# Performance work log

Hardware: AMD Instinct MI355X
Metric: run time of the kernel (lower is better)

## Reference

```python
import jax, jax.numpy as jnp
import numpy as np

EPS = 1e-12  # torch F.normalize default eps


def setup_inputs() -> dict:
    key = jax.random.key(0)
    ks = jax.random.split(key, 4)
    b, c, h, w = 2, 192, 256, 256
    num_heads = 4
    x = jax.random.normal(ks[0], (b, c, h, w), dtype=jnp.float32)
    w_qkv = jax.random.normal(ks[1], (3 * c, c), dtype=jnp.float32) * 0.02
    w_dw = jax.random.normal(ks[2], (3 * c, 1, 3, 3), dtype=jnp.float32) * 0.1
    w_proj = jax.random.normal(ks[3], (c, c), dtype=jnp.float32) * 0.02
    temperature = jnp.ones((num_heads, 1, 1), dtype=jnp.float32)
    return {"x": x, "w_qkv": w_qkv, "w_dw": w_dw, "w_proj": w_proj,
            "temperature": temperature, "num_heads": num_heads}


def reference(x, w_qkv, w_dw, w_proj, temperature, num_heads):
    b, c, h, w = x.shape
    ch = c // num_heads
    # 1x1 conv (pointwise GEMM) then depthwise 3x3 conv
    qkv = jnp.einsum('bchw,oc->bohw', x, w_qkv)
    qkv = jax.lax.conv_general_dilated(
        qkv, w_dw, window_strides=(1, 1), padding='SAME',
        dimension_numbers=('NCHW', 'OIHW', 'NCHW'),
        feature_group_count=3 * c)
    q, k, v = jnp.split(qkv, 3, axis=1)
    # b (head c) h w -> b head (c h) w
    def to_heads(t):
        return t.reshape(b, num_heads, ch * h, w)
    q, k, v = to_heads(q), to_heads(k), to_heads(v)
    # L2-normalize over the (c h) axis
    def l2n(t):
        n = jnp.sqrt(jnp.sum(t * t, axis=-2, keepdims=True))
        return t / jnp.maximum(n, EPS)
    q, k = l2n(q), l2n(k)
    # channel-transposed attention over width: attn is (b, head, w, w)
    attn = jnp.einsum('bhcw,bhcv->bhwv', q, k) * temperature[None]
    attn = jax.nn.softmax(attn, axis=-2)  # softmax over dim=-2 as in source
    out = jnp.einsum('bhcw,bhwv->bhcv', v, attn)
    out = out.reshape(b, c, h, w)
    return jnp.einsum('bchw,oc->bohw', out, w_proj)
```

## Files before the change

kernel.cpp:

```cpp
#include <hip/hip_runtime.h>
#include <math.h>

#define HW 65536

typedef float f32x4 __attribute__((ext_vector_type(4)));
typedef short bf16x8 __attribute__((ext_vector_type(8)));
typedef short bf16x4 __attribute__((ext_vector_type(4)));

static constexpr size_t OFF_A0    = 0;
static constexpr size_t OFF_SP    = 100663296;
static constexpr size_t OFF_QKT   = 150994944;
static constexpr size_t OFF_VPL   = 251658240;
static constexpr size_t OFF_PT    = 301989888;
static constexpr size_t OFF_NORMS = 303038464;
static constexpr size_t OFF_WQ    = 303054848;
static constexpr size_t OFF_WP    = 303276032;

__device__ inline float b2f(unsigned short u) { union { unsigned u; float f; } v; v.u = ((unsigned)u) << 16; return v.f; }
__device__ inline unsigned short f2b(float f) {
    union { float f; unsigned u; } v; v.f = f;
    return (unsigned short)((v.u + 0x7fffu + ((v.u >> 16) & 1u)) >> 16);
}

__global__ __launch_bounds__(256) void conv_w(const float* __restrict__ wq, const float* __restrict__ wp,
                                              unsigned short* __restrict__ wqb, unsigned short* __restrict__ wpb)
{
    int t = blockIdx.x * 256 + threadIdx.x;
    int stride = gridDim.x * 256;
    for (int i = t; i < 576 * 192; i += stride) wqb[i] = f2b(wq[i]);
    for (int i = t; i < 192 * 192; i += stride) wpb[i] = f2b(wp[i]);
}

template <int MODE>
__global__ __launch_bounds__(256) void gemm_pm5(const unsigned short* __restrict__ Aw,
                                                const void* __restrict__ Bsrc,
                                                unsigned short* __restrict__ outb,
                                                float* __restrict__ outf, int Mtiles)
{
    __shared__ unsigned short Bs[192 * 130];
    int tid = threadIdx.x;
    int w = tid >> 6, lane = tid & 63, lg = lane >> 4, li = lane & 15;
    int wm = w >> 1, wn = w & 1;
    const int b = (int)(blockIdx.x >> 9);
    const long px0 = (long)(blockIdx.x & 511) * 128;

    if (MODE == 0) {
        const float* X = (const float*)Bsrc;
#pragma unroll
        for (int it = 0; it < 24; ++it) {
            int task = it * 256 + tid;
            int ch = task >> 5, seg = task & 31;
            float4 v = *(const float4*)(X + ((long)(b * 192 + ch)) * HW + px0 + seg * 4);
            unsigned* d32 = (unsigned*)&Bs[ch * 130 + seg * 4];
            d32[0] = (unsigned)f2b(v.x) | ((unsigned)f2b(v.y) << 16);
            d32[1] = (unsigned)f2b(v.z) | ((unsigned)f2b(v.w) << 16);
        }
    } else {
        const unsigned short* X = (const unsigned short*)Bsrc;
#pragma unroll
        for (int it = 0; it < 12; ++it) {
            int task = it * 256 + tid;
            int ch = task >> 4, seg = task & 15;
            bf16x8 v = *(const bf16x8*)(X + ((long)(b * 192 + ch)) * HW + px0 + seg * 8);
            unsigned* d32 = (unsigned*)&Bs[ch * 130 + seg * 8];
            const unsigned* s32 = (const unsigned*)&v;
            d32[0] = s32[0]; d32[1] = s32[1]; d32[2] = s32[2]; d32[3] = s32[3];
        }
    }
    __syncthreads();

    bf16x8 Bf[4][6];
#pragma unroll
    for (int fb = 0; fb < 4; ++fb) {
        int px = wn * 64 + fb * 16 + li;
#pragma unroll
        for (int ks = 0; ks < 6; ++ks) {
            bf16x8 v;
#pragma unroll
            for (int e = 0; e < 8; ++e)
                v[e] = (short)Bs[(ks * 32 + lg * 8 + e) * 130 + px];
            Bf[fb][ks] = v;
        }
    }
    __syncthreads();

    float* Ls32 = (float*)Bs;
    const int wbase = w * 1088;
    const int pxw = (int)px0 + wn * 64;
    const int Mtot = Mtiles * 64;
    const int r = lane >> 2, q = lane & 3;

    for (int mt = 0; mt < Mtiles; ++mt) {
        int oc0 = mt * 64;
        const unsigned short* ab = Aw + (long)(oc0 + wm * 32 + li) * 192 + lg * 8;
        f32x4 acc[2][4];
#pragma unroll
        for (int i = 0; i < 2; ++i)
#pragma unroll
            for (int j = 0; j < 4; ++j) acc[i][j] = (f32x4){0.f, 0.f, 0.f, 0.f};
#pragma unroll
        for (int ks = 0; ks < 6; ++ks) {
            bf16x8 a0 = *(const bf16x8*)(ab + ks * 32);
            bf16x8 a1 = *(const bf16x8*)(ab + 16 * 192 + ks * 32);
#pragma unroll
            for (int fb = 0; fb < 4; ++fb) {
                acc[0][fb] = __builtin_amdgcn_mfma_f32_16x16x32_bf16(a0, Bf[fb][ks], acc[0][fb], 0, 0, 0);
                acc[1][fb] = __builtin_amdgcn_mfma_f32_16x16x32_bf16(a1, Bf[fb][ks], acc[1][fb], 0, 0, 0);
            }
        }
#pragma unroll
        for (int fa = 0; fa < 2; ++fa) {
#pragma unroll
            for (int fb = 0; fb < 4; ++fb)
#pragma unroll
                for (int ii = 0; ii < 4; ++ii)
                    Ls32[wbase + (lg * 4 + ii) * 68 + fb * 16 + li] = acc[fa][fb][ii];
            f32x4 c0 = *(f32x4*)&Ls32[wbase + r * 68 + q * 16 + 0];
            f32x4 c1 = *(f32x4*)&Ls32[wbase + r * 68 + q * 16 + 4];
            f32x4 c2 = *(f32x4*)&Ls32[wbase + r * 68 + q * 16 + 8];
            f32x4 c3 = *(f32x4*)&Ls32[wbase + r * 68 + q * 16 + 12];
            int m = oc0 + wm * 32 + fa * 16 + r;
            long base = ((long)b * Mtot + m) * HW + pxw + q * 16;
            if (MODE == 1) {
                *(f32x4*)(outf + base + 0)  = c0;
                *(f32x4*)(outf + base + 4)  = c1;
                *(f32x4*)(outf + base + 8)  = c2;
                *(f32x4*)(outf + base + 12) = c3;
            } else {
                bf16x8 o0, o1;
#pragma unroll
                for (int e = 0; e < 4; ++e) {
                    o0[e]     = (short)f2b(c0[e]);
                    o0[e + 4] = (short)f2b(c1[e]);
                    o1[e]     = (short)f2b(c2[e]);
                    o1[e + 4] = (short)f2b(c3[e]);
                }
                *(bf16x8*)(outb + base)     = o0;
                *(bf16x8*)(outb + base + 8) = o1;
            }
        }
    }
}

__global__ __launch_bounds__(256) void dwconv2(const unsigned short* __restrict__ in,
                                               const float* __restrict__ wdw,
                                               unsigned short* __restrict__ qkT,
                                               unsigned short* __restrict__ vpl)
{
    __shared__ unsigned short Ls[34 * 272];
    int tid = threadIdx.x;
    int zp = blockIdx.y;
    int b = zp / 576, ch3 = zp % 576;
    int y0 = blockIdx.x * 32;
    const unsigned short* ip = in + (long)zp * HW;
    float w9[9];
#pragma unroll
    for (int t = 0; t < 9; ++t) w9[t] = wdw[ch3 * 9 + t];

    const bf16x8 z8 = (bf16x8){0, 0, 0, 0, 0, 0, 0, 0};
    if (tid < 34)               *(bf16x8*)&Ls[tid * 272] = z8;
    else if (tid < 68)          *(bf16x8*)&Ls[(tid - 34) * 272 + 264] = z8;
#pragma unroll
    for (int it = 0; it < 5; ++it) {
        int task = it * 256 + tid;
        if (task < 1088) {
            int r = task >> 5, seg = task & 31;
            int gy = y0 - 1 + r;
            bf16x8 v = z8;
            if (gy >= 0 && gy < 256) v = *(const bf16x8*)(ip + gy * 256 + seg * 8);
            *(bf16x8*)&Ls[r * 272 + 8 + seg * 8] = v;
        }
    }
    __syncthreads();

    int xg = tid & 63, yg = tid >> 6;
    int x0 = xg * 4;
    float acc[8][4];
#pragma unroll
    for (int yy = 0; yy < 8; ++yy)
#pragma unroll
        for (int xi = 0; xi < 4; ++xi) acc[yy][xi] = 0.f;

#pragma unroll
    for (int rr = 0; rr < 10; ++rr) {
        const unsigned short* lp = &Ls[(yg * 8 + rr) * 272 + 8 + x0];
        bf16x4 A  = *(const bf16x4*)(lp - 4);
        bf16x4 Bv = *(const bf16x4*)(lp);
        bf16x4 Cv = *(const bf16x4*)(lp + 4);
        float f[6] = { b2f((unsigned short)A[3]),  b2f((unsigned short)Bv[0]),
                       b2f((unsigned short)Bv[1]), b2f((unsigned short)Bv[2]),
                       b2f((unsigned short)Bv[3]), b2f((unsigned short)Cv[0]) };
#pragma unroll
        for (int dy = 0; dy < 3; ++dy) {
            int yy = rr - dy;
            if (yy >= 0 && yy < 8) {
#pragma unroll
                for (int dx = 0; dx < 3; ++dx)
#pragma unroll
                    for (int xi = 0; xi < 4; ++xi)
                        acc[yy][xi] = fmaf(w9[dy * 3 + dx], f[dx + xi], acc[yy][xi]);
            }
        }
    }

    if (ch3 < 384) {
        int isk = ch3 >= 192 ? 1 : 0;
        int chq = ch3 - isk * 192;
        int hh = chq / 48, cc = chq % 48;
        long zbase = (long)(b * 8 + isk * 4 + hh) * 3145728L + (long)cc * 256 + y0 + yg * 8;
#pragma unroll
        for (int xi = 0; xi < 4; ++xi) {
            bf16x8 pv;
#pragma unroll
            for (int yy = 0; yy < 8; ++yy) pv[yy] = (short)f2b(acc[yy][xi]);
            *(bf16x8*)(qkT + zbase + (long)(x0 + xi) * 12288) = pv;
        }
    } else {
        unsigned short* ob = vpl + (long)(b * 192 + ch3 - 384) * HW + (long)(y0 + yg * 8) * 256 + x0;
#pragma unroll
        for (int yy = 0; yy < 8; ++yy) {
            bf16x4 pv;
#pragma unroll
            for (int xi = 0; xi < 4; ++xi) pv[xi] = (short)f2b(acc[yy][xi]);
            *(bf16x4*)(ob + yy * 256) = pv;
        }
    }
}

__global__ __launch_bounds__(256) void norms_k(const unsigned short* __restrict__ qkT, float* __restrict__ norms)
{
    int i = blockIdx.x, z = blockIdx.y;
    const unsigned short* p = qkT + ((long)z * 256 + i) * 12288 + threadIdx.x * 8;
    float s = 0.f;
#pragma unroll
    for (int it = 0; it < 6; ++it) {
        bf16x8 v = *(const bf16x8*)(p + it * 2048);
#pragma unroll
        for (int e = 0; e < 8; ++e) { float f = b2f((unsigned short)v[e]); s = fmaf(f, f, s); }
    }
    for (int off = 32; off > 0; off >>= 1) s += __shfl_down(s, off, 64);
    __shared__ float r4[4];
    if ((threadIdx.x & 63) == 0) r4[threadIdx.x >> 6] = s;
    __syncthreads();
    if (threadIdx.x == 0) {
        float t = r4[0] + r4[1] + r4[2] + r4[3];
        norms[z * 256 + i] = 1.0f / fmaxf(sqrtf(t), 1e-12f);
    }
}

__global__ __launch_bounds__(256) void attn_qk(const unsigned short* __restrict__ qkT, float* __restrict__ Sp)
{
    __shared__ unsigned short Qs[128 * 40];
    __shared__ unsigned short Ks[128 * 40];
    int tid = threadIdx.x;
    int z = blockIdx.z; int bh = z >> 4, sk = z & 15; int b = bh >> 2, h = bh & 3;
    const unsigned short* qT = qkT + (long)(b * 8 + h) * 3145728;
    const unsigned short* kT = qkT + (long)(b * 8 + 4 + h) * 3145728;
    int i0 = blockIdx.x * 128, j0 = blockIdx.y * 128;
    int w = tid >> 6, lane = tid & 63, lg = lane >> 4, li = lane & 15;
    int wm = w >> 1, wn = w & 1;
    int srow = tid >> 2, sseg = (tid & 3) * 8;
    long qoff = (long)(i0 + srow) * 12288 + sk * 768 + sseg;
    long koff = (long)(j0 + srow) * 12288 + sk * 768 + sseg;

    f32x4 acc[4][4];
#pragma unroll
    for (int i = 0; i < 4; ++i)
#pragma unroll
        for (int j = 0; j < 4; ++j) acc[i][j] = (f32x4){0.f, 0.f, 0.f, 0.f};

    bf16x8 qr0 = *(const bf16x8*)(qT + qoff);
    bf16x8 qr1 = *(const bf16x8*)(qT + qoff + (long)64 * 12288);
    bf16x8 kr0 = *(const bf16x8*)(kT + koff);
    bf16x8 kr1 = *(const bf16x8*)(kT + koff + (long)64 * 12288);

#pragma unroll 1
    for (int ks = 0; ks < 24; ++ks) {
        *(bf16x8*)&Qs[srow * 40 + sseg] = qr0;
        *(bf16x8*)&Qs[(64 + srow) * 40 + sseg] = qr1;
        *(bf16x8*)&Ks[srow * 40 + sseg] = kr0;
        *(bf16x8*)&Ks[(64 + srow) * 40 + sseg] = kr1;
        if (ks < 23) {
            long o = (long)(ks + 1) * 32;
            qr0 = *(const bf16x8*)(qT + qoff + o);
            qr1 = *(const bf16x8*)(qT + qoff + (long)64 * 12288 + o);
            kr0 = *(const bf16x8*)(kT + koff + o);
            kr1 = *(const bf16x8*)(kT + koff + (long)64 * 12288 + o);
        }
        __syncthreads();
        bf16x8 af[4], bfr[4];
#pragma unroll
        for (int fa = 0; fa < 4; ++fa)
            af[fa] = *(const bf16x8*)&Qs[(wm * 64 + fa * 16 + li) * 40 + lg * 8];
#pragma unroll
        for (int fb = 0; fb < 4; ++fb)
            bfr[fb] = *(const bf16x8*)&Ks[(wn * 64 + fb * 16 + li) * 40 + lg * 8];
#pragma unroll
        for (int fa = 0; fa < 4; ++fa)
#pragma unroll
            for (int fb = 0; fb < 4; ++fb)
                acc[fa][fb] = __builtin_amdgcn_mfma_f32_16x16x32_bf16(af[fa], bfr[fb], acc[fa][fb], 0, 0, 0);
        __syncthreads();
    }

    float* op = Sp + ((long)(sk * 8 + bh) << 16);
#pragma unroll
    for (int fa = 0; fa < 4; ++fa) {
        int i = i0 + wm * 64 + fa * 16 + lg * 4;
#pragma unroll
        for (int fb = 0; fb < 4; ++fb) {
            int j = j0 + wn * 64 + fb * 16 + li;
#pragma unroll
            for (int ii = 0; ii < 4; ++ii)
                op[(long)(i + ii) * 256 + j] = acc[fa][fb][ii];
        }
    }
}

__global__ __launch_bounds__(256) void softmax_k(const float* __restrict__ Sp, const float* __restrict__ norms,
                                                 const float* __restrict__ temp, unsigned short* __restrict__ Pt)
{
    __shared__ float Sd[256 * 9];
    __shared__ float red[32 * 9];
    int tid = threadIdx.x;
    int g = blockIdx.x; int bh = g >> 5, jq = g & 31; int b = bh >> 2, h = bh & 3;
    int jl = tid & 7, iq = tid >> 3;
    int j = jq * 8 + jl;
    const float* nq = norms + (b * 8 + h) * 256;
    float invkj = norms[(b * 8 + 4 + h) * 256 + j] * temp[h];
    const float* sp = Sp + (long)bh * HW + j;

    float m = -1e30f;
#pragma unroll
    for (int ii = 0; ii < 8; ++ii) {
        int i = iq * 8 + ii;
        float s = 0.f;
#pragma unroll
        for (int sk = 0; sk < 16; ++sk) s += sp[((long)(sk * 8) << 16) + i * 256];
        float v = s * nq[i] * invkj;
        Sd[i * 9 + jl] = v;
        m = fmaxf(m, v);
    }
    red[iq * 9 + jl] = m;
    __syncthreads();
    m = -1e30f;
#pragma unroll
    for (int s2 = 0; s2 < 32; ++s2) m = fmaxf(m, red[s2 * 9 + jl]);
    __syncthreads();
    float sum = 0.f;
#pragma unroll
    for (int ii = 0; ii < 8; ++ii) sum += __expf(Sd[(iq * 8 + ii) * 9 + jl] - m);
    red[iq * 9 + jl] = sum;
    __syncthreads();
    sum = 0.f;
#pragma unroll
    for (int s2 = 0; s2 < 32; ++s2) sum += red[s2 * 9 + jl];
    float rs = 1.0f / sum;

    int fb = jq >> 1, li2 = (jq & 1) * 8 + jl;
    int ks = iq >> 2, lg = iq & 3;
    unsigned short* pt = Pt + (long)bh * HW + (long)((fb * 8 + ks) * 64 + lg * 16 + li2) * 8;
    bf16x8 pv;
#pragma unroll
    for (int ii = 0; ii < 8; ++ii)
        pv[ii] = (short)f2b(__expf(Sd[(iq * 8 + ii) * 9 + jl] - m) * rs);
    *(bf16x8*)pt = pv;
}

__global__ __launch_bounds__(256) void vattn(const unsigned short* __restrict__ vpl,
                                             const unsigned short* __restrict__ Pt,
                                             unsigned short* __restrict__ vout)
{
    int tid = threadIdx.x;
    int w = tid >> 6, lane = tid & 63, lg = lane >> 4, li = lane & 15;
    int wm = w >> 1, wn = w & 1;
    int m0 = blockIdx.x * 64 + wm * 32;
    int bh = blockIdx.y; int b = bh >> 2, h = bh & 3;
    const unsigned short* V = vpl + (long)(b * 192 + h * 48) * HW;
    const unsigned short* P = Pt + (long)bh * HW + wn * 32768 + lane * 8;

    f32x4 acc[2][8];
#pragma unroll
    for (int i = 0; i < 2; ++i)
#pragma unroll
        for (int j = 0; j < 8; ++j) acc[i][j] = (f32x4){0.f, 0.f, 0.f, 0.f};

#pragma unroll 2
    for (int ks = 0; ks < 8; ++ks) {
        bf16x8 a0 = *(const bf16x8*)(V + (long)(m0 + li) * 256 + ks * 32 + lg * 8);
        bf16x8 a1 = *(const bf16x8*)(V + (long)(m0 + 16 + li) * 256 + ks * 32 + lg * 8);
#pragma unroll
        for (int fb2 = 0; fb2 < 8; ++fb2) {
            bf16x8 bb = *(const bf16x8*)(P + (fb2 * 8 + ks) * 512);
            acc[0][fb2] = __builtin_amdgcn_mfma_f32_16x16x32_bf16(a0, bb, acc[0][fb2], 0, 0, 0);
            acc[1][fb2] = __builtin_amdgcn_mfma_f32_16x16x32_bf16(a1, bb, acc[1][fb2], 0, 0, 0);
        }
    }
    unsigned short* ob = vout + (long)(b * 192 + h * 48) * HW;
#pragma unroll
    for (int fa = 0; fa < 2; ++fa) {
#pragma unroll
        for (int fb2 = 0; fb2 < 8; ++fb2) {
            int j = (wn * 8 + fb2) * 16 + li;
#pragma unroll
            for (int ii = 0; ii < 4; ++ii) {
                int m = m0 + fa * 16 + lg * 4 + ii;
                ob[((long)(m >> 8) << 16) + ((m & 255) << 8) + j] = f2b(acc[fa][fb2][ii]);
            }
        }
    }
}

extern "C" void kernel_launch(void* const* d_in, const int* in_sizes, int n_in,
                              void* d_out, int out_size, void* d_ws, size_t ws_size,
                              hipStream_t stream)
{
    (void)in_sizes; (void)n_in; (void)out_size; (void)ws_size;
    const float* x      = (const float*)d_in[0];
    const float* w_qkv  = (const float*)d_in[1];
    const float* w_dw   = (const float*)d_in[2];
    const float* w_proj = (const float*)d_in[3];
    const float* temp   = (const float*)d_in[4];
    float* out = (float*)d_out;
    char* ws = (char*)d_ws;

    unsigned short* qkv_pre = (unsigned short*)(ws + OFF_A0);
    float*          Sp      = (float*)(ws + OFF_SP);
    unsigned short* vout    = (unsigned short*)(ws + OFF_A0);
    unsigned short* qkT     = (unsigned short*)(ws + OFF_QKT);
    unsigned short* vpl     = (unsigned short*)(ws + OFF_VPL);
    unsigned short* Pt      = (unsigned short*)(ws + OFF_PT);
    float*          norms   = (float*)(ws + OFF_NORMS);
    unsigned short* wqb     = (unsigned short*)(ws + OFF_WQ);
    unsigned short* wpb     = (unsigned short*)(ws + OFF_WP);

    conv_w<<<64, 256, 0, stream>>>(w_qkv, w_proj, wqb, wpb);
    gemm_pm5<0><<<1024, 256, 0, stream>>>(wqb, (const void*)x, qkv_pre, nullptr, 9);
    dwconv2<<<dim3(8, 1152), 256, 0, stream>>>(qkv_pre, w_dw, qkT, vpl);
    norms_k<<<dim3(256, 16), 256, 0, stream>>>(qkT, norms);
    attn_qk<<<dim3(2, 2, 128), 256, 0, stream>>>(qkT, Sp);
    softmax_k<<<256, 256, 0, stream>>>(Sp, norms, temp, Pt);
    vattn<<<dim3(192, 8), 256, 0, stream>>>(vpl, Pt, vout);
    gemm_pm5<1><<<1024, 256, 0, stream>>>(wpb, (const void*)vout, nullptr, out, 3);
}
```

Before: 332.9 us.

## Pre-transpose GEMM B operands to pixel-major bf16 and load fragments directly

Adds a conv_x kernel that converts x to bf16 in pixel-major (HWC) layout, and a transpose kernel that does the same for the attention output, so the pointwise GEMMs can load B fragments straight from global memory. This drops the LDS staging and the scalar, strided LDS gathers used to build the fragments. In exchange it adds two extra passes over large tensors (about 50MB of x read plus 25MB written, and a transposed copy of vout), plus extra launches. The workspace offsets are reshuffled so the new buffers fit.

```diff
diff --git a/kernel.cpp b/kernel.cpp
--- a/kernel.cpp
+++ b/kernel.cpp
@@ -8,8 +8,9 @@
 typedef short bf16x4 __attribute__((ext_vector_type(4)));
 
 static constexpr size_t OFF_A0    = 0;
-static constexpr size_t OFF_SP    = 100663296;
-static constexpr size_t OFF_QKT   = 150994944;
+static constexpr size_t OFF_SP    = 50331648;
+static constexpr size_t OFF_VOUTT = 100663296;
+static constexpr size_t OFF_XQK   = 150994944;
 static constexpr size_t OFF_VPL   = 251658240;
 static constexpr size_t OFF_PT    = 301989888;
 static constexpr size_t OFF_NORMS = 303038464;
@@ -31,60 +32,51 @@
     for (int i = t; i < 192 * 192; i += stride) wpb[i] = f2b(wp[i]);
 }
 
+__global__ __launch_bounds__(256) void conv_x(const float* __restrict__ x, unsigned short* __restrict__ xb)
+{
+    __shared__ unsigned short T[64 * 200];
+    int tid = threadIdx.x;
+    int b = blockIdx.y;
+    long p0 = (long)blockIdx.x * 64;
+#pragma unroll
+    for (int it = 0; it < 12; ++it) {
+        int c = it * 16 + (tid >> 4);
+        int px = (tid & 15) * 4;
+        float4 v = *(const float4*)(x + ((long)b * 192 + c) * HW + p0 + px);
+        T[(px + 0) * 200 + c] = f2b(v.x);
+        T[(px + 1) * 200 + c] = f2b(v.y);
+        T[(px + 2) * 200 + c] = f2b(v.z);
+        T[(px + 3) * 200 + c] = f2b(v.w);
+    }
+    __syncthreads();
+    int px = tid >> 2, q = tid & 3;
+    unsigned short* ob = xb + ((long)b * HW + p0 + px) * 192 + q * 48;
+#pragma unroll
+    for (int e = 0; e < 6; ++e)
+        *(bf16x8*)(ob + e * 8) = *(const bf16x8*)&T[px * 200 + q * 48 + e * 8];
+}
+
 template <int MODE>
-__global__ __launch_bounds__(256) void gemm_pm5(const unsigned short* __restrict__ Aw,
-                                                const void* __restrict__ Bsrc,
+__global__ __launch_bounds__(256) void gemm_pm6(const unsigned short* __restrict__ Aw,
+                                                const unsigned short* __restrict__ Bp,
                                                 unsigned short* __restrict__ outb,
                                                 float* __restrict__ outf, int Mtiles)
 {
-    __shared__ unsigned short Bs[192 * 130];
+    __shared__ float Ls32[4 * 1088];
     int tid = threadIdx.x;
     int w = tid >> 6, lane = tid & 63, lg = lane >> 4, li = lane & 15;
     int wm = w >> 1, wn = w & 1;
     const int b = (int)(blockIdx.x >> 9);
     const long px0 = (long)(blockIdx.x & 511) * 128;
 
-    if (MODE == 0) {
-        const float* X = (const float*)Bsrc;
-#pragma unroll
-        for (int it = 0; it < 24; ++it) {
-            int task = it * 256 + tid;
-            int ch = task >> 5, seg = task & 31;
-            float4 v = *(const float4*)(X + ((long)(b * 192 + ch)) * HW + px0 + seg * 4);
-            unsigned* d32 = (unsigned*)&Bs[ch * 130 + seg * 4];
-            d32[0] = (unsigned)f2b(v.x) | ((unsigned)f2b(v.y) << 16);
-            d32[1] = (unsigned)f2b(v.z) | ((unsigned)f2b(v.w) << 16);
-        }
-    } else {
-        const unsigned short* X = (const unsigned short*)Bsrc;
-#pragma unroll
-        for (int it = 0; it < 12; ++it) {
-            int task = it * 256 + tid;
-            int ch = task >> 4, seg = task & 15;
-            bf16x8 v = *(const bf16x8*)(X + ((long)(b * 192 + ch)) * HW + px0 + seg * 8);
-            unsigned* d32 = (unsigned*)&Bs[ch * 130 + seg * 8];
-            const unsigned* s32 = (const unsigned*)&v;
-            d32[0] = s32[0]; d32[1] = s32[1]; d32[2] = s32[2]; d32[3] = s32[3];
-        }
-    }
-    __syncthreads();
-
+    const unsigned short* bb = Bp + ((long)b * HW + px0 + wn * 64 + li) * 192 + lg * 8;
     bf16x8 Bf[4][6];
 #pragma unroll
-    for (int fb = 0; fb < 4; ++fb) {
-        int px = wn * 64 + fb * 16 + li;
-#pragma unroll
-        for (int ks = 0; ks < 6; ++ks) {
-            bf16x8 v;
-#pragma unroll
-            for (int e = 0; e < 8; ++e)
-                v[e] = (short)Bs[(ks * 32 + lg * 8 + e) * 130 + px];
-            Bf[fb][ks] = v;
-        }
-    }
-    __syncthreads();
-
-    float* Ls32 = (float*)Bs;
+    for (int fb = 0; fb < 4; ++fb)
+#pragma unroll
+        for (int ks = 0; ks < 6; ++ks)
+            Bf[fb][ks] = *(const bf16x8*)(bb + (long)fb * 16 * 192 + ks * 32);
+
     const int wbase = w * 1088;
     const int pxw = (int)px0 + wn * 64;
     const int Mtot = Mtiles * 64;
@@ -227,6 +219,42 @@
     }
 }
 
+__global__ __launch_bounds__(256) void transpose_bf16(const unsigned short* __restrict__ src,
+                                                      unsigned short* __restrict__ dst, int mode)
+{
+    __shared__ unsigned short T[64][72];
+    int tid = threadIdx.x;
+    int z = blockIdx.z;
+    long so, dofs; int R, C;
+    if (mode == 0) {
+        int b = z >> 3, isk = (z >> 2) & 1, h = z & 3;
+        so = ((long)(b * 576 + isk * 192 + h * 48)) * HW;
+        dofs = (long)z * 12288 * 256;
+        R = 12288; C = 256;
+    } else {
+        so = (long)z * 192 * HW;
+        dofs = (long)z * HW * 192;
+        R = 192; C = HW;
+    }
+    int r0 = blockIdx.y * 64, c0 = blockIdx.x * 64;
+#pragma unroll
+    for (int rr = 0; rr < 2; ++rr) {
+        int r = rr * 32 + (tid >> 3);
+        int cs = (tid & 7) * 8;
+        *(bf16x8*)&T[r][cs] = *(const bf16x8*)(src + so + (long)(r0 + r) * C + c0 + cs);
+    }
+    __syncthreads();
+#pragma unroll
+    for (int cc = 0; cc < 2; ++cc) {
+        int c = cc * 32 + (tid >> 3);
+        int rs = (tid & 7) * 8;
+        bf16x8 v;
+#pragma unroll
+        for (int e = 0; e < 8; ++e) v[e] = (short)T[rs + e][c];
+        *(bf16x8*)(dst + dofs + (long)(c0 + c) * R + r0 + rs) = v;
+    }
+}
+
 __global__ __launch_bounds__(256) void norms_k(const unsigned short* __restrict__ qkT, float* __restrict__ norms)
 {
     int i = blockIdx.x, z = blockIdx.y;
@@ -425,9 +453,11 @@
     char* ws = (char*)d_ws;
 
     unsigned short* qkv_pre = (unsigned short*)(ws + OFF_A0);
+    unsigned short* vout    = (unsigned short*)(ws + OFF_A0);
     float*          Sp      = (float*)(ws + OFF_SP);
-    unsigned short* vout    = (unsigned short*)(ws + OFF_A0);
-    unsigned short* qkT     = (unsigned short*)(ws + OFF_QKT);
+    unsigned short* voutT   = (unsigned short*)(ws + OFF_VOUTT);
+    unsigned short* xb      = (unsigned short*)(ws + OFF_XQK);
+    unsigned short* qkT     = (unsigned short*)(ws + OFF_XQK);
     unsigned short* vpl     = (unsigned short*)(ws + OFF_VPL);
     unsigned short* Pt      = (unsigned short*)(ws + OFF_PT);
     float*          norms   = (float*)(ws + OFF_NORMS);
@@ -435,11 +465,13 @@
     unsigned short* wpb     = (unsigned short*)(ws + OFF_WP);
 
     conv_w<<<64, 256, 0, stream>>>(w_qkv, w_proj, wqb, wpb);
-    gemm_pm5<0><<<1024, 256, 0, stream>>>(wqb, (const void*)x, qkv_pre, nullptr, 9);
+    conv_x<<<dim3(1024, 2), 256, 0, stream>>>(x, xb);
+    gemm_pm6<0><<<1024, 256, 0, stream>>>(wqb, xb, qkv_pre, nullptr, 9);
     dwconv2<<<dim3(8, 1152), 256, 0, stream>>>(qkv_pre, w_dw, qkT, vpl);
     norms_k<<<dim3(256, 16), 256, 0, stream>>>(qkT, norms);
     attn_qk<<<dim3(2, 2, 128), 256, 0, stream>>>(qkT, Sp);
     softmax_k<<<256, 256, 0, stream>>>(Sp, norms, temp, Pt);
     vattn<<<dim3(192, 8), 256, 0, stream>>>(vpl, Pt, vout);
-    gemm_pm5<1><<<1024, 256, 0, stream>>>(wpb, (const void*)vout, nullptr, out, 3);
-}
+    transpose_bf16<<<dim3(1024, 3, 2), 256, 0, stream>>>(vout, voutT, 1);
+    gemm_pm6<1><<<1024, 256, 0, stream>>>(wpb, voutT, nullptr, out, 3);
+}
```

After: 392.1 us. 17.8% more time.
